# Kernel optimization log

Measured on AMD Instinct MI355X. Metric: run time of the kernel, lower is better.

## Reference

```python
import jax, jax.numpy as jnp
import numpy as np

N, H, F = 131072, 256, 4096
MIN_FRAG = 3
LN_EPS = 1e-5
NORM_EPS = 1e-12
CONSISTENCY_FACTOR = 0.03
INTERMOLECULAR_WEIGHT = 0.2
SCALING_FACTOR = 0.05  # initial_strength at epoch 0 (progressive schedule, eval mode)


def _normalize(x):
    # torch F.normalize(p=2, dim=1): x / max(||x||, eps)
    n = jnp.linalg.norm(x, axis=-1, keepdims=True)
    return x / jnp.maximum(n, NORM_EPS)


def _frag_consistency(feat, frag_ids, valid):
    # size-weighted sum of per-fragment mean deviations == mean deviation over valid atoms
    m = valid.astype(feat.dtype)[:, None]
    seg_sum = jax.ops.segment_sum(feat * m, frag_ids, num_segments=F)
    seg_cnt = jax.ops.segment_sum(m, frag_ids, num_segments=F)
    means = seg_sum / jnp.maximum(seg_cnt, 1.0)  # scatter-mean over valid atoms
    sim = jnp.sum(_normalize(feat) * _normalize(means)[frag_ids], axis=-1)  # [N]
    dev = (1.0 - sim) * valid.astype(feat.dtype)
    return jnp.sum(dev) / jnp.maximum(jnp.sum(valid.astype(feat.dtype)), 1.0)


def setup_inputs() -> dict:
    key = jax.random.key(0)
    ks = jax.random.split(key, 8)
    return {
        "scalar_short": jax.random.normal(ks[0], (N, H), jnp.float32),
        "scalar_long": jax.random.normal(ks[1], (N, H), jnp.float32),
        "vector_short": jax.random.normal(ks[2], (N, 3, H), jnp.float32),
        "vector_long": jax.random.normal(ks[3], (N, 3, H), jnp.float32),
        "fragment_ids": jax.random.randint(ks[4], (N,), 0, F, dtype=jnp.int32),
        "ln_gamma": jnp.ones((H,), jnp.float32),
        "ln_beta": jnp.zeros((H,), jnp.float32),
        "W1": jax.random.normal(ks[5], (H, H), jnp.float32) / np.sqrt(H),
        "b1": jnp.zeros((H,), jnp.float32),
        "Wv": jax.random.normal(ks[6], (H, H), jnp.float32) / np.sqrt(H),
    }


def reference(scalar_short, scalar_long, vector_short, vector_long, fragment_ids,
              ln_gamma, ln_beta, W1, b1, Wv):
    # valid_mask: atoms belonging to fragments of size >= MIN_FRAG
    sizes = jax.ops.segment_sum(jnp.ones((N,), jnp.float32), fragment_ids, num_segments=F)
    valid = sizes[fragment_ids] >= MIN_FRAG  # [N] bool

    # scalar_projector: LayerNorm -> Linear -> SiLU (dropout identity at eval)
    mu = jnp.mean(scalar_short, axis=-1, keepdims=True)
    var = jnp.var(scalar_short, axis=-1, keepdims=True)
    xh = (scalar_short - mu) / jnp.sqrt(var + LN_EPS) * ln_gamma + ln_beta
    scalar_features = jax.nn.silu(xh @ W1.T + b1)  # [N, H]

    intra = _frag_consistency(scalar_features, fragment_ids, valid)

    # vector branch: per-atom magnitude = mean over 3 spatial comps of ||.||_2 over hidden
    vec_mag = jnp.mean(jnp.linalg.norm(vector_short, axis=2), axis=1, keepdims=True)  # [N,1]
    # Linear(bias=False) on mag.expand(-1,H) then [:, :1] == silu(mag * sum(Wv[0,:]))
    w0 = jnp.sum(Wv[0])
    vector_features = jax.nn.silu(vec_mag * w0)  # [N,1]
    vec_loss = _frag_consistency(vector_features, fragment_ids, valid)

    # interfragment differentiation over ALL atoms (no valid mask)
    cnt = jax.ops.segment_sum(jnp.ones((N, 1), jnp.float32), fragment_ids, num_segments=F)
    sfrag = jax.ops.segment_sum(scalar_features, fragment_ids, num_segments=F) / jnp.maximum(cnt, 1.0)
    vfrag = jax.ops.segment_sum(vec_mag, fragment_ids, num_segments=F) / jnp.maximum(cnt, 1.0)
    combined = _normalize(jnp.concatenate([sfrag, vfrag], axis=1))  # [F, H+1]
    sim = combined @ combined.T  # [F, F]
    off_sum = jnp.sum(sim) - jnp.trace(sim)
    inter = off_sum / (F * F - F + 1e-6)

    total = intra + vec_loss + INTERMOLECULAR_WEIGHT * inter
    return CONSISTENCY_FACTOR * total * SCALING_FACTOR
```

## Files before the change

### kernel.cpp

```cpp
#include <hip/hip_runtime.h>
#include <hip/hip_bf16.h>
#include <stdint.h>

#define NA 131072
#define HD 256
#define NF 4096
#define MINFRAG 3
#define LN_EPS 1e-5f
#define NEPS 1e-12f

#define OFF_CNT    0ull
#define OFF_VSUM   16384ull
#define OFF_VFSUM  32768ull
#define OFF_NVSUM  49152ull
#define OFF_FILL   65536ull
#define OFF_DBL    81920ull
#define OFF_SSUM   86016ull
#define OFF_NSUM   4280320ull
#define ZERO_BYTES 8474624ull
#define OFF_OFFS   8474624ull
#define OFF_SVEC   8491008ull
#define OFF_C0     8492032ull
#define OFF_W0     8493056ull
#define OFF_GBF    8493568ull
#define OFF_ORDER  8624640ull

#define IDX_TRACE 257
#define IDX_DEVS  258
#define IDX_DEVV  259
#define IDX_VCNT  260

typedef __attribute__((ext_vector_type(8))) short short8;
typedef __attribute__((ext_vector_type(4))) float f32x4;
union F4S8 { float4 f; short8 s; };
union BFU { __hip_bfloat16 b; unsigned short u; };

__device__ __forceinline__ unsigned short f2b(float x) {
    BFU t; t.b = __float2bfloat16(x); return t.u;
}
__device__ __forceinline__ float b2f(unsigned short u) {
    return __uint_as_float(((uint32_t)u) << 16);
}
__device__ __forceinline__ float silu_f(float x) {
    return x * __builtin_amdgcn_rcpf(1.f + __expf(-x));
}

__global__ __launch_bounds__(256) void k_zero(float4* __restrict__ z) {
    int i = blockIdx.x * 256 + threadIdx.x;
    float4 v = {0.f, 0.f, 0.f, 0.f};
    z[i] = v;
}

__global__ __launch_bounds__(256) void k_prep(
    const float* __restrict__ W1, const float* __restrict__ gamma,
    const float* __restrict__ beta, const float* __restrict__ b1,
    const float* __restrict__ Wv,
    unsigned short* __restrict__ Gbf, float* __restrict__ svec,
    float* __restrict__ c0, float* __restrict__ w0) {
    __shared__ float red[8];
    int o = blockIdx.x;
    int t = threadIdx.x;
    if (o < HD) {
        float w = W1[(size_t)o * HD + t];
        unsigned short gb = f2b(w * gamma[t]);
        Gbf[(size_t)o * HD + t] = gb;
        float sp = b2f(gb);
        float cp = w * beta[t];
#pragma unroll
        for (int m = 32; m; m >>= 1) { sp += __shfl_xor(sp, m, 64); cp += __shfl_xor(cp, m, 64); }
        int wv = t >> 6;
        if ((t & 63) == 0) { red[wv] = sp; red[4 + wv] = cp; }
        __syncthreads();
        if (t == 0) {
            svec[o] = red[0] + red[1] + red[2] + red[3];
            c0[o]   = red[4] + red[5] + red[6] + red[7] + b1[o];
        }
    } else {
        float v = Wv[t];
#pragma unroll
        for (int m = 32; m; m >>= 1) v += __shfl_xor(v, m, 64);
        int wv = t >> 6;
        if ((t & 63) == 0) red[wv] = v;
        __syncthreads();
        if (t == 0) w0[0] = red[0] + red[1] + red[2] + red[3];
    }
}

__global__ __launch_bounds__(256) void k_stats(
    const float* __restrict__ vs, const int* __restrict__ fid,
    const float* __restrict__ w0p,
    int* __restrict__ cnt, float* __restrict__ vsum,
    float* __restrict__ vfsum, float* __restrict__ nvsum) {
    int gwave = (blockIdx.x * blockDim.x + threadIdx.x) >> 6;
    int lane = threadIdx.x & 63;
    int nw = (gridDim.x * blockDim.x) >> 6;
    float w0 = w0p[0];
    for (int i0 = gwave * 2; i0 < NA; i0 += nw * 2) {
        const float* ba = vs + (size_t)i0 * 3 * HD;
        const float* bb = vs + (size_t)(i0 + 1) * 3 * HD;
        float4 a0 = ((const float4*)(ba))[lane];
        float4 a1 = ((const float4*)(ba + HD))[lane];
        float4 a2 = ((const float4*)(ba + 2 * HD))[lane];
        float4 b0 = ((const float4*)(bb))[lane];
        float4 b1 = ((const float4*)(bb + HD))[lane];
        float4 b2 = ((const float4*)(bb + 2 * HD))[lane];
        float qa0 = a0.x * a0.x + a0.y * a0.y + a0.z * a0.z + a0.w * a0.w;
        float qa1 = a1.x * a1.x + a1.y * a1.y + a1.z * a1.z + a1.w * a1.w;
        float qa2 = a2.x * a2.x + a2.y * a2.y + a2.z * a2.z + a2.w * a2.w;
        float qb0 = b0.x * b0.x + b0.y * b0.y + b0.z * b0.z + b0.w * b0.w;
        float qb1 = b1.x * b1.x + b1.y * b1.y + b1.z * b1.z + b1.w * b1.w;
        float qb2 = b2.x * b2.x + b2.y * b2.y + b2.z * b2.z + b2.w * b2.w;
#pragma unroll
        for (int m = 32; m; m >>= 1) {
            qa0 += __shfl_xor(qa0, m, 64);
            qa1 += __shfl_xor(qa1, m, 64);
            qa2 += __shfl_xor(qa2, m, 64);
            qb0 += __shfl_xor(qb0, m, 64);
            qb1 += __shfl_xor(qb1, m, 64);
            qb2 += __shfl_xor(qb2, m, 64);
        }
        if (lane == 0) {
            float vma = (sqrtf(qa0) + sqrtf(qa1) + sqrtf(qa2)) * (1.f / 3.f);
            float vmb = (sqrtf(qb0) + sqrtf(qb1) + sqrtf(qb2)) * (1.f / 3.f);
            float vfa = silu_f(vma * w0);
            float vfb = silu_f(vmb * w0);
            float nva = vfa / fmaxf(fabsf(vfa), NEPS);
            float nvb = vfb / fmaxf(fabsf(vfb), NEPS);
            int fa = fid[i0], fb = fid[i0 + 1];
            atomicAdd(&cnt[fa], 1);
            atomicAdd(&vsum[fa], vma);
            atomicAdd(&vfsum[fa], vfa);
            atomicAdd(&nvsum[fa], nva);
            atomicAdd(&cnt[fb], 1);
            atomicAdd(&vsum[fb], vmb);
            atomicAdd(&vfsum[fb], vfb);
            atomicAdd(&nvsum[fb], nvb);
        }
    }
}

__global__ __launch_bounds__(256) void k_scan(const int* __restrict__ cnt,
                                              int* __restrict__ offs) {
    __shared__ int wsum[4];
    int t = threadIdx.x;
    int base = t * 16;
    int c[16];
    int tot = 0;
#pragma unroll
    for (int j = 0; j < 16; ++j) { c[j] = cnt[base + j]; tot += c[j]; }
    int lane = t & 63, w = t >> 6;
    int v = tot;
#pragma unroll
    for (int d = 1; d < 64; d <<= 1) {
        int o = __shfl_up(v, d, 64);
        if (lane >= d) v += o;
    }
    if (lane == 63) wsum[w] = v;
    __syncthreads();
    int wbase = 0;
    for (int i = 0; i < w; ++i) wbase += wsum[i];
    int run = wbase + v - tot;
#pragma unroll
    for (int j = 0; j < 16; ++j) { offs[base + j] = run; run += c[j]; }
}

__global__ __launch_bounds__(256) void k_scatter(
    const int* __restrict__ fid, const int* __restrict__ offs,
    int* __restrict__ fill, int* __restrict__ order) {
    int i = blockIdx.x * blockDim.x + threadIdx.x;
    if (i < NA) {
        int f = fid[i];
        int p = atomicAdd(&fill[f], 1);
        order[offs[f] + p] = i;
    }
}

__global__ __launch_bounds__(256) void k_gemm(
    const float* __restrict__ A, const unsigned short* __restrict__ Gbf,
    const float* __restrict__ svec, const float* __restrict__ c0,
    const int* __restrict__ order, const int* __restrict__ fid,
    const int* __restrict__ offs, const int* __restrict__ cnt,
    float* __restrict__ ssum, float* __restrict__ nsum) {
    __shared__ float4 As16[64 * 32];
    __shared__ float muS[64], rsS[64], rnS[64];
    __shared__ float sqL[64][4];
    __shared__ int ridS[64], fragS[64];

    int tid = threadIdx.x;
    int lane = tid & 63, wid = tid >> 6;
    int r0 = blockIdx.x * 64;
    int rowT = tid >> 4;
    int c4 = tid & 15;

    if (tid < 64) {
        int gi = order[r0 + tid];
        ridS[tid] = gi;
        fragS[tid] = fid[gi];
    }
    __syncthreads();
    int rid[4];
#pragma unroll
    for (int p = 0; p < 4; ++p) rid[p] = ridS[16 * p + rowT];

    float s1p[4] = {0, 0, 0, 0}, s2p[4] = {0, 0, 0, 0};
#pragma unroll
    for (int kc = 0; kc < 4; ++kc)
#pragma unroll
        for (int p = 0; p < 4; ++p) {
            int row = 16 * p + rowT;
            float4 v = *(const float4*)(A + (size_t)rid[p] * HD + kc * 64 + c4 * 4);
            s1p[p] += v.x + v.y + v.z + v.w;
            s2p[p] += v.x * v.x + v.y * v.y + v.z * v.z + v.w * v.w;
            ushort4 pk;
            pk.x = f2b(v.x); pk.y = f2b(v.y); pk.z = f2b(v.z); pk.w = f2b(v.w);
            int slot = row * 32 + kc * 8 + ((c4 >> 1) ^ (row & 7));
            ((ushort4*)&As16[slot])[c4 & 1] = pk;
        }
#pragma unroll
    for (int p = 0; p < 4; ++p) {
        float s1 = s1p[p], s2 = s2p[p];
#pragma unroll
        for (int m = 1; m < 16; m <<= 1) {
            s1 += __shfl_xor(s1, m, 64);
            s2 += __shfl_xor(s2, m, 64);
        }
        if (c4 == 0) {
            int row = 16 * p + rowT;
            float mu_ = s1 * (1.f / HD);
            float var = s2 * (1.f / HD) - mu_ * mu_;
            muS[row] = mu_;
            rsS[row] = rsqrtf(var + LN_EPS);
        }
    }
    __syncthreads();

    int lg = lane >> 4;
    const unsigned short* bp[4];
#pragma unroll
    for (int ni = 0; ni < 4; ++ni)
        bp[ni] = Gbf + (size_t)(wid * 64 + ni * 16 + (lane & 15)) * HD + lg * 8;

    f32x4 acc[4][4] = {};
#pragma unroll
    for (int kc = 0; kc < 4; ++kc) {
        short8 bfr[2][4];
#pragma unroll
        for (int kk = 0; kk < 2; ++kk)
#pragma unroll
            for (int ni = 0; ni < 4; ++ni)
                bfr[kk][ni] = *(const short8*)(bp[ni] + kc * 64 + kk * 32);
#pragma unroll
        for (int kk = 0; kk < 2; ++kk) {
            int jp = kk * 4 + lg;
            short8 a[4];
#pragma unroll
            for (int mi = 0; mi < 4; ++mi) {
                int r = mi * 16 + (lane & 15);
                F4S8 t_; t_.f = As16[r * 32 + kc * 8 + (jp ^ (r & 7))];
                a[mi] = t_.s;
            }
#pragma unroll
            for (int mi = 0; mi < 4; ++mi)
#pragma unroll
                for (int ni = 0; ni < 4; ++ni)
                    acc[mi][ni] = __builtin_amdgcn_mfma_f32_16x16x32_bf16(
                        a[mi], bfr[kk][ni], acc[mi][ni], 0, 0, 0);
        }
    }
    __syncthreads();

    float sv[4], cv[4];
#pragma unroll
    for (int ni = 0; ni < 4; ++ni) {
        int c = wid * 64 + ni * 16 + (lane & 15);
        sv[ni] = svec[c];
        cv[ni] = c0[c];
    }
    unsigned short* featS = (unsigned short*)As16;
    float sq[4][4];
#pragma unroll
    for (int mi = 0; mi < 4; ++mi)
#pragma unroll
        for (int q = 0; q < 4; ++q) {
            int rl = mi * 16 + (lane >> 4) * 4 + q;
            float mu_ = muS[rl], rs_ = rsS[rl];
            float sqa = 0.f;
#pragma unroll
            for (int ni = 0; ni < 4; ++ni) {
                int c = wid * 64 + ni * 16 + (lane & 15);
                float pre = rs_ * (acc[mi][ni][q] - mu_ * sv[ni]) + cv[ni];
                unsigned short us = f2b(silu_f(pre));
                featS[rl * 256 + (c ^ ((rl & 7) << 2))] = us;
                float fr = b2f(us);
                sqa += fr * fr;
            }
            sq[mi][q] = sqa;
        }
#pragma unroll
    for (int mi = 0; mi < 4; ++mi)
#pragma unroll
        for (int q = 0; q < 4; ++q) {
            float s_ = sq[mi][q];
            s_ += __shfl_xor(s_, 1, 64);
            s_ += __shfl_xor(s_, 2, 64);
            s_ += __shfl_xor(s_, 4, 64);
            s_ += __shfl_xor(s_, 8, 64);
            if ((lane & 15) == 0) sqL[mi * 16 + (lane >> 4) * 4 + q][wid] = s_;
        }
    __syncthreads();
    if (tid < 64) {
        float t = sqL[tid][0] + sqL[tid][1] + sqL[tid][2] + sqL[tid][3];
        rnS[tid] = 1.f / fmaxf(sqrtf(t), NEPS);
    }
    __syncthreads();
    int cc = wid * 64 + lane;
    float sAcc = 0.f, nAcc = 0.f;
    int curF = fragS[0];
    for (int row = 0; row < 64; ++row) {
        int f = fragS[row];
        if (f != curF) {
            int gs = offs[curF], n = cnt[curF];
            if (gs >= r0 && gs + n <= r0 + 64) {
                ssum[(size_t)curF * HD + cc] = sAcc;
                nsum[(size_t)curF * HD + cc] = nAcc;
            } else {
                atomicAdd(&ssum[(size_t)curF * HD + cc], sAcc);
                atomicAdd(&nsum[(size_t)curF * HD + cc], nAcc);
            }
            sAcc = 0.f; nAcc = 0.f; curF = f;
        }
        float v = b2f(featS[row * 256 + (cc ^ ((row & 7) << 2))]);
        sAcc += v;
        nAcc = fmaf(v, rnS[row], nAcc);
    }
    {
        int gs = offs[curF], n = cnt[curF];
        if (gs >= r0 && gs + n <= r0 + 64) {
            ssum[(size_t)curF * HD + cc] = sAcc;
            nsum[(size_t)curF * HD + cc] = nAcc;
        } else {
            atomicAdd(&ssum[(size_t)curF * HD + cc], sAcc);
            atomicAdd(&nsum[(size_t)curF * HD + cc], nAcc);
        }
    }
}

__global__ __launch_bounds__(256) void k_frag(
    const float* __restrict__ ssum, const float* __restrict__ nsum,
    const int* __restrict__ cnt, const float* __restrict__ vsum,
    const float* __restrict__ vfsum, const float* __restrict__ nvsum,
    double* __restrict__ dbl) {
    int gwave = (blockIdx.x * blockDim.x + threadIdx.x) >> 6;
    int lane = threadIdx.x & 63;
    int nw = (gridDim.x * blockDim.x) >> 6;

    double la0 = 0, la1 = 0, la2 = 0, la3 = 0;
    double lv = 0, ltr = 0, lvc = 0, ldS = 0, ldV = 0;

    for (int f = gwave; f < NF; f += nw) {
        float4 s = ((const float4*)(ssum + (size_t)f * HD))[lane];
        float4 nn = ((const float4*)(nsum + (size_t)f * HD))[lane];
        int c = cnt[f];
        float ssq = s.x * s.x + s.y * s.y + s.z * s.z + s.w * s.w;
        float dsn = nn.x * s.x + nn.y * s.y + nn.z * s.z + nn.w * s.w;
#pragma unroll
        for (int m = 32; m; m >>= 1) {
            ssq += __shfl_xor(ssq, m, 64);
            dsn += __shfl_xor(dsn, m, 64);
        }
        float inv_all = 1.f / fmaxf((float)c, 1.f);
        float m0 = s.x * inv_all, m1 = s.y * inv_all, m2 = s.z * inv_all, m3 = s.w * inv_all;
        float ssq_mean = ssq * inv_all * inv_all;
        float vfr = vsum[f] * inv_all;
        float nrm2 = ssq_mean + vfr * vfr;
        float inv = 1.f / fmaxf(sqrtf(nrm2), NEPS);
        la0 += (double)(m0 * inv);
        la1 += (double)(m1 * inv);
        la2 += (double)(m2 * inv);
        la3 += (double)(m3 * inv);
        if (lane == 0) {
            lv += (double)(vfr * inv);
            ltr += (double)(nrm2 * inv * inv);
            if (c >= MINFRAG) {
                lvc += (double)c;
                float denom = fmaxf(sqrtf(ssq), NEPS);
                ldS += (double)c - (double)(dsn / denom);
                float vfm = vfsum[f] * inv_all;
                float vsgn = vfm / fmaxf(fabsf(vfm), NEPS);
                ldV += (double)c - (double)(vsgn * nvsum[f]);
            }
        }
    }
    atomicAdd(&dbl[4 * lane + 0], la0);
    atomicAdd(&dbl[4 * lane + 1], la1);
    atomicAdd(&dbl[4 * lane + 2], la2);
    atomicAdd(&dbl[4 * lane + 3], la3);
    if (lane == 0) {
        atomicAdd(&dbl[256], lv);
        atomicAdd(&dbl[IDX_TRACE], ltr);
        atomicAdd(&dbl[IDX_VCNT], lvc);
        atomicAdd(&dbl[IDX_DEVS], ldS);
        atomicAdd(&dbl[IDX_DEVV], ldV);
    }
}

__global__ __launch_bounds__(64) void k_final(const double* __restrict__ dbl,
                                              float* __restrict__ out) {
    if (threadIdx.x == 0 && blockIdx.x == 0) {
        double s2 = 0;
        for (int d = 0; d < 257; ++d) s2 += dbl[d] * dbl[d];
        double off = s2 - dbl[IDX_TRACE];
        double inter = off / ((double)NF * NF - NF + 1e-6);
        double vc = fmax(dbl[IDX_VCNT], 1.0);
        double total = dbl[IDX_DEVS] / vc + dbl[IDX_DEVV] / vc + 0.2 * inter;
        out[0] = (float)(0.03 * 0.05 * total);
    }
}

extern "C" void kernel_launch(void* const* d_in, const int* in_sizes, int n_in,
                              void* d_out, int out_size, void* d_ws, size_t ws_size,
                              hipStream_t stream) {
    const float* scalar_short = (const float*)d_in[0];
    const float* vector_short = (const float*)d_in[2];
    const int* fragment_ids = (const int*)d_in[4];
    const float* ln_gamma = (const float*)d_in[5];
    const float* ln_beta = (const float*)d_in[6];
    const float* W1 = (const float*)d_in[7];
    const float* b1 = (const float*)d_in[8];
    const float* Wv = (const float*)d_in[9];
    float* out = (float*)d_out;

    char* ws = (char*)d_ws;
    int* cnt = (int*)(ws + OFF_CNT);
    float* vsum = (float*)(ws + OFF_VSUM);
    float* vfsum = (float*)(ws + OFF_VFSUM);
    float* nvsum = (float*)(ws + OFF_NVSUM);
    int* fill = (int*)(ws + OFF_FILL);
    double* dbl = (double*)(ws + OFF_DBL);
    float* ssum = (float*)(ws + OFF_SSUM);
    float* nsum = (float*)(ws + OFF_NSUM);
    int* offs = (int*)(ws + OFF_OFFS);
    float* svec = (float*)(ws + OFF_SVEC);
    float* c0 = (float*)(ws + OFF_C0);
    float* w0 = (float*)(ws + OFF_W0);
    unsigned short* Gbf = (unsigned short*)(ws + OFF_GBF);
    int* order = (int*)(ws + OFF_ORDER);

    k_zero<<<2069, 256, 0, stream>>>((float4*)ws);
    k_prep<<<HD + 1, 256, 0, stream>>>(W1, ln_gamma, ln_beta, b1, Wv, Gbf, svec, c0, w0);
    k_stats<<<2048, 256, 0, stream>>>(vector_short, fragment_ids, w0, cnt, vsum, vfsum, nvsum);
    k_scan<<<1, 256, 0, stream>>>(cnt, offs);
    k_scatter<<<NA / 256, 256, 0, stream>>>(fragment_ids, offs, fill, order);
    k_gemm<<<NA / 64, 256, 0, stream>>>(scalar_short, Gbf, svec, c0, order,
                                        fragment_ids, offs, cnt, ssum, nsum);
    k_frag<<<64, 256, 0, stream>>>(ssum, nsum, cnt, vsum, vfsum, nvsum, dbl);
    k_final<<<1, 64, 0, stream>>>(dbl, out);
}
```

Baseline: 250.7 us.

## Fuse vector-magnitude stats into GEMM kernel and split out atom histogram

```diff
diff --git a/kernel.cpp b/kernel.cpp
--- a/kernel.cpp
+++ b/kernel.cpp
@@ -86,57 +86,10 @@
     }
 }
 
-__global__ __launch_bounds__(256) void k_stats(
-    const float* __restrict__ vs, const int* __restrict__ fid,
-    const float* __restrict__ w0p,
-    int* __restrict__ cnt, float* __restrict__ vsum,
-    float* __restrict__ vfsum, float* __restrict__ nvsum) {
-    int gwave = (blockIdx.x * blockDim.x + threadIdx.x) >> 6;
-    int lane = threadIdx.x & 63;
-    int nw = (gridDim.x * blockDim.x) >> 6;
-    float w0 = w0p[0];
-    for (int i0 = gwave * 2; i0 < NA; i0 += nw * 2) {
-        const float* ba = vs + (size_t)i0 * 3 * HD;
-        const float* bb = vs + (size_t)(i0 + 1) * 3 * HD;
-        float4 a0 = ((const float4*)(ba))[lane];
-        float4 a1 = ((const float4*)(ba + HD))[lane];
-        float4 a2 = ((const float4*)(ba + 2 * HD))[lane];
-        float4 b0 = ((const float4*)(bb))[lane];
-        float4 b1 = ((const float4*)(bb + HD))[lane];
-        float4 b2 = ((const float4*)(bb + 2 * HD))[lane];
-        float qa0 = a0.x * a0.x + a0.y * a0.y + a0.z * a0.z + a0.w * a0.w;
-        float qa1 = a1.x * a1.x + a1.y * a1.y + a1.z * a1.z + a1.w * a1.w;
-        float qa2 = a2.x * a2.x + a2.y * a2.y + a2.z * a2.z + a2.w * a2.w;
-        float qb0 = b0.x * b0.x + b0.y * b0.y + b0.z * b0.z + b0.w * b0.w;
-        float qb1 = b1.x * b1.x + b1.y * b1.y + b1.z * b1.z + b1.w * b1.w;
-        float qb2 = b2.x * b2.x + b2.y * b2.y + b2.z * b2.z + b2.w * b2.w;
-#pragma unroll
-        for (int m = 32; m; m >>= 1) {
-            qa0 += __shfl_xor(qa0, m, 64);
-            qa1 += __shfl_xor(qa1, m, 64);
-            qa2 += __shfl_xor(qa2, m, 64);
-            qb0 += __shfl_xor(qb0, m, 64);
-            qb1 += __shfl_xor(qb1, m, 64);
-            qb2 += __shfl_xor(qb2, m, 64);
-        }
-        if (lane == 0) {
-            float vma = (sqrtf(qa0) + sqrtf(qa1) + sqrtf(qa2)) * (1.f / 3.f);
-            float vmb = (sqrtf(qb0) + sqrtf(qb1) + sqrtf(qb2)) * (1.f / 3.f);
-            float vfa = silu_f(vma * w0);
-            float vfb = silu_f(vmb * w0);
-            float nva = vfa / fmaxf(fabsf(vfa), NEPS);
-            float nvb = vfb / fmaxf(fabsf(vfb), NEPS);
-            int fa = fid[i0], fb = fid[i0 + 1];
-            atomicAdd(&cnt[fa], 1);
-            atomicAdd(&vsum[fa], vma);
-            atomicAdd(&vfsum[fa], vfa);
-            atomicAdd(&nvsum[fa], nva);
-            atomicAdd(&cnt[fb], 1);
-            atomicAdd(&vsum[fb], vmb);
-            atomicAdd(&vfsum[fb], vfb);
-            atomicAdd(&nvsum[fb], nvb);
-        }
-    }
+__global__ __launch_bounds__(256) void k_hist(
+    const int* __restrict__ fid, int* __restrict__ cnt) {
+    int i = blockIdx.x * 256 + threadIdx.x;
+    if (i < NA) atomicAdd(&cnt[fid[i]], 1);
 }
 
 __global__ __launch_bounds__(256) void k_scan(const int* __restrict__ cnt,
@@ -178,8 +131,11 @@
 __global__ __launch_bounds__(256) void k_gemm(
     const float* __restrict__ A, const unsigned short* __restrict__ Gbf,
     const float* __restrict__ svec, const float* __restrict__ c0,
+    const float* __restrict__ vs, const float* __restrict__ w0p,
     const int* __restrict__ order, const int* __restrict__ fid,
     const int* __restrict__ offs, const int* __restrict__ cnt,
+    float* __restrict__ vsum, float* __restrict__ vfsum,
+    float* __restrict__ nvsum,
     float* __restrict__ ssum, float* __restrict__ nsum) {
     __shared__ float4 As16[64 * 32];
     __shared__ float muS[64], rsS[64], rnS[64];
@@ -341,6 +297,53 @@
         } else {
             atomicAdd(&ssum[(size_t)curF * HD + cc], sAcc);
             atomicAdd(&nsum[(size_t)curF * HD + cc], nAcc);
+        }
+    }
+
+    {
+        float w0 = w0p[0];
+#pragma unroll 1
+        for (int j = 0; j < 16; j += 2) {
+            int lr0 = wid * 16 + j, lr1 = lr0 + 1;
+            int gia = ridS[lr0], gib = ridS[lr1];
+            const float* ba = vs + (size_t)gia * 3 * HD;
+            const float* bb = vs + (size_t)gib * 3 * HD;
+            float4 a0 = ((const float4*)(ba))[lane];
+            float4 a1 = ((const float4*)(ba + HD))[lane];
+            float4 a2 = ((const float4*)(ba + 2 * HD))[lane];
+            float4 b0 = ((const float4*)(bb))[lane];
+            float4 b1 = ((const float4*)(bb + HD))[lane];
+            float4 b2 = ((const float4*)(bb + 2 * HD))[lane];
+            float qa0 = a0.x * a0.x + a0.y * a0.y + a0.z * a0.z + a0.w * a0.w;
+            float qa1 = a1.x * a1.x + a1.y * a1.y + a1.z * a1.z + a1.w * a1.w;
+            float qa2 = a2.x * a2.x + a2.y * a2.y + a2.z * a2.z + a2.w * a2.w;
+            float qb0 = b0.x * b0.x + b0.y * b0.y + b0.z * b0.z + b0.w * b0.w;
+            float qb1 = b1.x * b1.x + b1.y * b1.y + b1.z * b1.z + b1.w * b1.w;
+            float qb2 = b2.x * b2.x + b2.y * b2.y + b2.z * b2.z + b2.w * b2.w;
+#pragma unroll
+            for (int m = 32; m; m >>= 1) {
+                qa0 += __shfl_xor(qa0, m, 64);
+                qa1 += __shfl_xor(qa1, m, 64);
+                qa2 += __shfl_xor(qa2, m, 64);
+                qb0 += __shfl_xor(qb0, m, 64);
+                qb1 += __shfl_xor(qb1, m, 64);
+                qb2 += __shfl_xor(qb2, m, 64);
+            }
+            if (lane == 0) {
+                float vma = (sqrtf(qa0) + sqrtf(qa1) + sqrtf(qa2)) * (1.f / 3.f);
+                float vmb = (sqrtf(qb0) + sqrtf(qb1) + sqrtf(qb2)) * (1.f / 3.f);
+                float vfa = silu_f(vma * w0);
+                float vfb = silu_f(vmb * w0);
+                float nva = vfa / fmaxf(fabsf(vfa), NEPS);
+                float nvb = vfb / fmaxf(fabsf(vfb), NEPS);
+                int fa = fragS[lr0], fb = fragS[lr1];
+                atomicAdd(&vsum[fa], vma);
+                atomicAdd(&vfsum[fa], vfa);
+                atomicAdd(&nvsum[fa], nva);
+                atomicAdd(&vsum[fb], vmb);
+                atomicAdd(&vfsum[fb], vfb);
+                atomicAdd(&nvsum[fb], nvb);
+            }
         }
     }
 }
@@ -448,11 +451,12 @@
 
     k_zero<<<2069, 256, 0, stream>>>((float4*)ws);
     k_prep<<<HD + 1, 256, 0, stream>>>(W1, ln_gamma, ln_beta, b1, Wv, Gbf, svec, c0, w0);
-    k_stats<<<2048, 256, 0, stream>>>(vector_short, fragment_ids, w0, cnt, vsum, vfsum, nvsum);
+    k_hist<<<NA / 256, 256, 0, stream>>>(fragment_ids, cnt);
     k_scan<<<1, 256, 0, stream>>>(cnt, offs);
     k_scatter<<<NA / 256, 256, 0, stream>>>(fragment_ids, offs, fill, order);
-    k_gemm<<<NA / 64, 256, 0, stream>>>(scalar_short, Gbf, svec, c0, order,
-                                        fragment_ids, offs, cnt, ssum, nsum);
+    k_gemm<<<NA / 64, 256, 0, stream>>>(scalar_short, Gbf, svec, c0,
+                                        vector_short, w0, order, fragment_ids,
+                                        offs, cnt, vsum, vfsum, nvsum, ssum, nsum);
     k_frag<<<64, 256, 0, stream>>>(ssum, nsum, cnt, vsum, vfsum, nvsum, dbl);
     k_final<<<1, 64, 0, stream>>>(dbl, out);
 }
```

Result: slower. 275.3 us (+9.8%).

## Fuse zeroing into prep and replace fp64 atomics with block partial reduction

Applied to the files above, without the earlier changes.

```diff
diff --git a/kernel.cpp b/kernel.cpp
--- a/kernel.cpp
+++ b/kernel.cpp
@@ -24,11 +24,14 @@
 #define OFF_W0     8493056ull
 #define OFF_GBF    8493568ull
 #define OFF_ORDER  8624640ull
+#define OFF_PART   9150464ull
 
 #define IDX_TRACE 257
 #define IDX_DEVS  258
 #define IDX_DEVV  259
 #define IDX_VCNT  260
+#define FRAGB 256
+#define PSTRIDE 264
 
 typedef __attribute__((ext_vector_type(8))) short short8;
 typedef __attribute__((ext_vector_type(4))) float f32x4;
@@ -43,12 +46,6 @@
 }
 __device__ __forceinline__ float silu_f(float x) {
     return x * __builtin_amdgcn_rcpf(1.f + __expf(-x));
-}
-
-__global__ __launch_bounds__(256) void k_zero(float4* __restrict__ z) {
-    int i = blockIdx.x * 256 + threadIdx.x;
-    float4 v = {0.f, 0.f, 0.f, 0.f};
-    z[i] = v;
 }
 
 __global__ __launch_bounds__(256) void k_prep(
@@ -56,10 +53,14 @@
     const float* __restrict__ beta, const float* __restrict__ b1,
     const float* __restrict__ Wv,
     unsigned short* __restrict__ Gbf, float* __restrict__ svec,
-    float* __restrict__ c0, float* __restrict__ w0) {
+    float* __restrict__ c0, float* __restrict__ w0, float4* __restrict__ z) {
     __shared__ float red[8];
     int o = blockIdx.x;
     int t = threadIdx.x;
+    {
+        float4 zv = {0.f, 0.f, 0.f, 0.f};
+        z[o * 256 + t] = zv;
+    }
     if (o < HD) {
         float w = W1[(size_t)o * HD + t];
         unsigned short gb = f2b(w * gamma[t]);
@@ -75,7 +76,7 @@
             svec[o] = red[0] + red[1] + red[2] + red[3];
             c0[o]   = red[4] + red[5] + red[6] + red[7] + b1[o];
         }
-    } else {
+    } else if (o == HD) {
         float v = Wv[t];
 #pragma unroll
         for (int m = 32; m; m >>= 1) v += __shfl_xor(v, m, 64);
@@ -349,10 +350,12 @@
     const float* __restrict__ ssum, const float* __restrict__ nsum,
     const int* __restrict__ cnt, const float* __restrict__ vsum,
     const float* __restrict__ vfsum, const float* __restrict__ nvsum,
-    double* __restrict__ dbl) {
-    int gwave = (blockIdx.x * blockDim.x + threadIdx.x) >> 6;
-    int lane = threadIdx.x & 63;
-    int nw = (gridDim.x * blockDim.x) >> 6;
+    double* __restrict__ partial) {
+    __shared__ double lred[4][PSTRIDE];
+    int tid = threadIdx.x;
+    int lane = tid & 63, wid = tid >> 6;
+    int gwave = blockIdx.x * 4 + wid;
+    const int nw = FRAGB * 4;
 
     double la0 = 0, la1 = 0, la2 = 0, la3 = 0;
     double lv = 0, ltr = 0, lvc = 0, ldS = 0, ldV = 0;
@@ -391,28 +394,40 @@
             }
         }
     }
-    atomicAdd(&dbl[4 * lane + 0], la0);
-    atomicAdd(&dbl[4 * lane + 1], la1);
-    atomicAdd(&dbl[4 * lane + 2], la2);
-    atomicAdd(&dbl[4 * lane + 3], la3);
+    lred[wid][4 * lane + 0] = la0;
+    lred[wid][4 * lane + 1] = la1;
+    lred[wid][4 * lane + 2] = la2;
+    lred[wid][4 * lane + 3] = la3;
     if (lane == 0) {
-        atomicAdd(&dbl[256], lv);
-        atomicAdd(&dbl[IDX_TRACE], ltr);
-        atomicAdd(&dbl[IDX_VCNT], lvc);
-        atomicAdd(&dbl[IDX_DEVS], ldS);
-        atomicAdd(&dbl[IDX_DEVV], ldV);
-    }
-}
-
-__global__ __launch_bounds__(64) void k_final(const double* __restrict__ dbl,
-                                              float* __restrict__ out) {
-    if (threadIdx.x == 0 && blockIdx.x == 0) {
+        lred[wid][256] = lv;
+        lred[wid][IDX_TRACE] = ltr;
+        lred[wid][IDX_DEVS] = ldS;
+        lred[wid][IDX_DEVV] = ldV;
+        lred[wid][IDX_VCNT] = lvc;
+    }
+    __syncthreads();
+    for (int idx = tid; idx < 261; idx += 256)
+        partial[(size_t)blockIdx.x * PSTRIDE + idx] =
+            lred[0][idx] + lred[1][idx] + lred[2][idx] + lred[3][idx];
+}
+
+__global__ __launch_bounds__(256) void k_final(const double* __restrict__ partial,
+                                               float* __restrict__ out) {
+    __shared__ double fin[PSTRIDE];
+    int t = threadIdx.x;
+    for (int idx = t; idx < 261; idx += 256) {
+        double s = 0;
+        for (int b = 0; b < FRAGB; ++b) s += partial[(size_t)b * PSTRIDE + idx];
+        fin[idx] = s;
+    }
+    __syncthreads();
+    if (t == 0) {
         double s2 = 0;
-        for (int d = 0; d < 257; ++d) s2 += dbl[d] * dbl[d];
-        double off = s2 - dbl[IDX_TRACE];
+        for (int d = 0; d < 257; ++d) s2 += fin[d] * fin[d];
+        double off = s2 - fin[IDX_TRACE];
         double inter = off / ((double)NF * NF - NF + 1e-6);
-        double vc = fmax(dbl[IDX_VCNT], 1.0);
-        double total = dbl[IDX_DEVS] / vc + dbl[IDX_DEVV] / vc + 0.2 * inter;
+        double vc = fmax(fin[IDX_VCNT], 1.0);
+        double total = fin[IDX_DEVS] / vc + fin[IDX_DEVV] / vc + 0.2 * inter;
         out[0] = (float)(0.03 * 0.05 * total);
     }
 }
@@ -436,7 +451,6 @@
     float* vfsum = (float*)(ws + OFF_VFSUM);
     float* nvsum = (float*)(ws + OFF_NVSUM);
     int* fill = (int*)(ws + OFF_FILL);
-    double* dbl = (double*)(ws + OFF_DBL);
     float* ssum = (float*)(ws + OFF_SSUM);
     float* nsum = (float*)(ws + OFF_NSUM);
     int* offs = (int*)(ws + OFF_OFFS);
@@ -445,14 +459,15 @@
     float* w0 = (float*)(ws + OFF_W0);
     unsigned short* Gbf = (unsigned short*)(ws + OFF_GBF);
     int* order = (int*)(ws + OFF_ORDER);
-
-    k_zero<<<2069, 256, 0, stream>>>((float4*)ws);
-    k_prep<<<HD + 1, 256, 0, stream>>>(W1, ln_gamma, ln_beta, b1, Wv, Gbf, svec, c0, w0);
+    double* partial = (double*)(ws + OFF_PART);
+
+    k_prep<<<2069, 256, 0, stream>>>(W1, ln_gamma, ln_beta, b1, Wv, Gbf, svec,
+                                     c0, w0, (float4*)ws);
     k_stats<<<2048, 256, 0, stream>>>(vector_short, fragment_ids, w0, cnt, vsum, vfsum, nvsum);
     k_scan<<<1, 256, 0, stream>>>(cnt, offs);
     k_scatter<<<NA / 256, 256, 0, stream>>>(fragment_ids, offs, fill, order);
     k_gemm<<<NA / 64, 256, 0, stream>>>(scalar_short, Gbf, svec, c0, order,
                                         fragment_ids, offs, cnt, ssum, nsum);
-    k_frag<<<64, 256, 0, stream>>>(ssum, nsum, cnt, vsum, vfsum, nvsum, dbl);
-    k_final<<<1, 64, 0, stream>>>(dbl, out);
-}
+    k_frag<<<FRAGB, 256, 0, stream>>>(ssum, nsum, cnt, vsum, vfsum, nvsum, partial);
+    k_final<<<1, 256, 0, stream>>>(partial, out);
+}
```

Measured after the change: 226.7 us. -9.6%, faster.
